# Kernel tuning notes

Measured on AMD Instinct MI355X. Metric: run time of the kernel, lower is better.

Reference implementation:

```python
import jax, jax.numpy as jnp
import numpy as np

B, N, C, K = 8, 4096, 128, 20  # batch, points-per-cloud, channels (n_cout), knn neighbors
NEG_SLOPE = 0.01  # torch F.leaky_relu default


def setup_inputs() -> dict:
    key = jax.random.key(0)
    ks = jax.random.split(key, 6)
    s = 1.0 / np.sqrt(C).astype(np.float32)
    xyz = jax.random.normal(ks[0], (B, 3, N), jnp.float32)
    points = jax.random.normal(ks[1], (B, C, N), jnp.float32)
    Wc = jax.random.normal(ks[2], (C, C), jnp.float32) * s  # center 1x1 conv weight (out,in)
    bc = jax.random.normal(ks[3], (C,), jnp.float32) * s
    Wg = jax.random.normal(ks[4], (C, C), jnp.float32) * s  # grouped 1x1 conv weight
    bg = jax.random.normal(ks[5], (C,), jnp.float32) * s
    return {"xyz": xyz, "points": points, "Wc": Wc, "bc": bc, "Wg": Wg, "bg": bg}


def reference(xyz, points, Wc, bc, Wg, bg):
    # xyz: [B,3,N], points: [B,C,N]
    k = K
    shortcut = points
    p = jax.nn.leaky_relu(points, NEG_SLOPE)        # [B,C,N]
    pt = jnp.transpose(p, (0, 2, 1))                # [B,N,C]
    xt = jnp.transpose(xyz, (0, 2, 1))              # [B,N,3]

    # pairwise squared distances [B,N,N]
    sq_norm = jnp.sum(xt * xt, axis=-1)             # [B,N]
    sq = sq_norm[:, :, None] - 2.0 * jnp.einsum('bnd,bmd->bnm', xt, xt) + sq_norm[:, None, :]

    # knn: k+1 nearest (incl. self), drop self -> [B,N,k]
    _, idx = jax.lax.top_k(-sq, k + 1)
    idx = idx[:, :, 1:]

    # gather neighbor features: [B,N,k,C]
    grouped = jax.vmap(lambda a, i: a[i])(pt, idx)

    # center 1x1 conv on [B,C,1,N] == per-point linear
    center = jnp.einsum('oc,bcn->bon', Wc, p) + bc[None, :, None]      # [B,C,N]
    # grouped 1x1 conv on [B,C,k,N]
    gout = jnp.einsum('oc,bnkc->bokn', Wg, grouped) + bg[None, :, None, None]  # [B,C,k,N]

    # mean over concat([center(1), grouped(k)], axis=2) then residual
    pooled = (center + jnp.sum(gout, axis=2)) / (k + 1)
    return pooled + shortcut
```

## Files before the change

### kernel.cpp

```cpp
#include <hip/hip_runtime.h>

#define B 8
#define N 4096
#define C 128
#define C2 256
#define KNN 21
#define CAP 22

typedef unsigned long long u64;
typedef unsigned int u32;
typedef unsigned short u16;

typedef __attribute__((ext_vector_type(8))) short bf16x8;
typedef __attribute__((ext_vector_type(4))) float f32x4;

__device__ __forceinline__ float bf2f(u16 u) {
    return __uint_as_float(((u32)u) << 16);
}
__device__ __forceinline__ u16 f2bf(float f) {
    u32 x = __float_as_uint(f);
    return (u16)((x + 0x7FFFu + ((x >> 16) & 1u)) >> 16);
}

__global__ __launch_bounds__(256) void k_transpose_lrelu(
        const float* __restrict__ pts, u16* __restrict__ X) {
    __shared__ u16 tile[32][33];
    int b  = blockIdx.z;
    int c0 = blockIdx.y * 32;
    int n0 = blockIdx.x * 32;
    int tx = threadIdx.x, ty = threadIdx.y;
    const float* src = pts + (size_t)b * C * N;
    #pragma unroll
    for (int i = 0; i < 32; i += 8) {
        float v = src[(size_t)(c0 + ty + i) * N + n0 + tx];
        if (v < 0.f) v = __fmul_rn(v, 0.01f);
        tile[ty + i][tx] = f2bf(v);
    }
    __syncthreads();
    u16* dst = X + (size_t)b * N * C2;
    #pragma unroll
    for (int i = 0; i < 32; i += 8) {
        dst[(size_t)(n0 + ty + i) * C2 + (c0 + tx)] = tile[tx][ty + i];
    }
}

__global__ __launch_bounds__(256) void k_pack_w(
        const float* __restrict__ Wc, const float* __restrict__ Wg,
        u16* __restrict__ Wt) {
    int e = blockIdx.x * 256 + threadIdx.x;
    int o = e >> 8, c = e & 255;
    float v = (c < 128) ? Wc[o * 128 + c] : Wg[o * 128 + (c - 128)];
    Wt[e] = f2bf(v);
}

__global__ __launch_bounds__(256) void k_knn_gather(
        const float* __restrict__ xyz, u16* __restrict__ X) {
    __shared__ __align__(16) char lds[61440];
    float4* stg = (float4*)lds;
    u64*    buf = (u64*)(lds + 16384);
    u64*    mg  = (u64*)lds;
    __shared__ u16 win[64 * KNN];

    int tid = threadIdx.x;
    int w = tid >> 6, l = tid & 63;
    int b = blockIdx.y;
    int n0 = blockIdx.x * 64;
    int nq = n0 + l;

    const float* xz = xyz + (size_t)b * 3 * N;
    float qx = xz[nq], qy = xz[N + nq], qz = xz[2 * N + nq];
    float snq = __fadd_rn(__fadd_rn(__fmul_rn(qx, qx), __fmul_rn(qy, qy)),
                          __fmul_rn(qz, qz));

    u64 slot[KNN];
    #pragma unroll
    for (int i = 0; i < KNN; ++i) slot[i] = ~0ull;
    int cnt = 0;
    u32 thr_kb = 0xFFFFFFFFu;
    float4* mystg = stg + w * 256;

    auto compact = [&]() {
        #pragma unroll 1
        for (int i = 0; i < CAP; ++i) {
            if (__ballot(i < cnt) == 0ull) break;
            u64 item = buf[i * 256 + tid];
            bool ins = (i < cnt) && (item < slot[20]);
            if (__ballot(ins) != 0ull) {
                u64 cnd = ins ? item : ~0ull;
                slot[20] = cnd < slot[20] ? cnd : slot[20];
                #pragma unroll
                for (int t = 19; t >= 0; --t) {
                    u64 a = slot[t], bb = slot[t + 1];
                    u64 lo = a < bb ? a : bb;
                    u64 hi = a < bb ? bb : a;
                    slot[t] = lo; slot[t + 1] = hi;
                }
            }
        }
        cnt = 0;
        thr_kb = (u32)(slot[20] >> 32);
    };

    for (int sc = 0; sc < 4; ++sc) {
        int m0 = w * 1024 + sc * 256;
        #pragma unroll
        for (int r = 0; r < 4; ++r) {
            int j = l + 64 * r, m = m0 + j;
            float x = xz[m], y = xz[N + m], z = xz[2 * N + m];
            float sn = __fadd_rn(__fadd_rn(__fmul_rn(x, x), __fmul_rn(y, y)),
                                 __fmul_rn(z, z));
            mystg[j] = make_float4(x, y, z, sn);
        }
        asm volatile("s_waitcnt lgkmcnt(0)" ::: "memory");
        for (int cc = 0; cc < 256; cc += 8) {
            #pragma unroll
            for (int j = 0; j < 8; ++j) {
                float4 cp = mystg[cc + j];
                int m = m0 + cc + j;
                float dot = __fadd_rn(__fadd_rn(__fmul_rn(qx, cp.x),
                                                __fmul_rn(qy, cp.y)),
                                      __fmul_rn(qz, cp.z));
                float sq = __fadd_rn(__fsub_rn(snq, __fadd_rn(dot, dot)), cp.w);
                u32 bits = __float_as_uint(sq);
                u32 kb = bits ^ (0x80000000u | (u32)(((int)bits) >> 31));
                buf[cnt * 256 + tid] = ((u64)kb << 32) | (u32)m;
                cnt += (kb <= thr_kb);
            }
            if (__ballot(cnt >= 15) != 0ull) compact();
        }
    }
    compact();

    __syncthreads();
    #pragma unroll
    for (int j = 0; j < KNN; ++j) mg[(w * 64 + l) * KNN + j] = slot[j];
    __syncthreads();

    if (w == 0) {
        int p0 = 0, p1 = 0, p2 = 0, p3 = 0;
        for (int j = 0; j < KNN; ++j) {
            u64 c0 = mg[(0 * 64 + l) * KNN + p0];
            u64 c1 = mg[(1 * 64 + l) * KNN + p1];
            u64 c2 = mg[(2 * 64 + l) * KNN + p2];
            u64 c3 = mg[(3 * 64 + l) * KNN + p3];
            u64 m01 = c0 < c1 ? c0 : c1; int s01 = c0 < c1 ? 0 : 1;
            u64 m23 = c2 < c3 ? c2 : c3; int s23 = c2 < c3 ? 2 : 3;
            u64 mm = m01 < m23 ? m01 : m23;
            int sel = m01 < m23 ? s01 : s23;
            win[l * KNN + j] = (u16)(mm & 0xFFFFu);
            p0 += (sel == 0); p1 += (sel == 1); p2 += (sel == 2); p3 += (sel == 3);
        }
    }
    __syncthreads();

    const u16* Xb = X + (size_t)b * N * C2;
    for (int qq = 0; qq < 16; ++qq) {
        int q = w * 16 + qq;
        float f0 = 0.f, f1 = 0.f;
        for (int j = 1; j < KNN; ++j) {
            int m = win[q * KNN + j];
            u32 u2 = *(const u32*)(Xb + (size_t)m * C2 + 2 * l);
            f0 += bf2f((u16)(u2 & 0xFFFFu));
            f1 += bf2f((u16)(u2 >> 16));
        }
        u16* dst = X + ((size_t)b * N + n0 + q) * C2 + 128 + 2 * l;
        *(u32*)dst = ((u32)f2bf(f1) << 16) | (u32)f2bf(f0);
    }
}

__global__ __launch_bounds__(256) void k_gemm_mfma(
        const u16* __restrict__ X, const u16* __restrict__ Wt,
        const float* __restrict__ pts, const float* __restrict__ bc,
        const float* __restrict__ bg, float* __restrict__ out) {
    int wid = blockIdx.x * 4 + (threadIdx.x >> 6);
    int lane = threadIdx.x & 63;
    int ot = wid & 7;
    int nt = wid >> 3;
    int b  = nt >> 6;
    int n0 = (nt & 63) * 64;

    int l16 = lane & 15, lq = lane >> 4;
    const u16* Xb = X + (size_t)b * N * C2;
    const u16* aptr = Wt + (size_t)(ot * 16 + l16) * C2 + lq * 8;
    const u16* bptr0 = Xb + (size_t)(n0 + 0 * 16 + l16) * C2 + lq * 8;
    const u16* bptr1 = Xb + (size_t)(n0 + 1 * 16 + l16) * C2 + lq * 8;
    const u16* bptr2 = Xb + (size_t)(n0 + 2 * 16 + l16) * C2 + lq * 8;
    const u16* bptr3 = Xb + (size_t)(n0 + 3 * 16 + l16) * C2 + lq * 8;

    f32x4 acc0 = {0.f, 0.f, 0.f, 0.f};
    f32x4 acc1 = {0.f, 0.f, 0.f, 0.f};
    f32x4 acc2 = {0.f, 0.f, 0.f, 0.f};
    f32x4 acc3 = {0.f, 0.f, 0.f, 0.f};
    #pragma unroll
    for (int kk = 0; kk < 8; ++kk) {
        bf16x8 a  = *(const bf16x8*)(aptr  + kk * 32);
        bf16x8 b0 = *(const bf16x8*)(bptr0 + kk * 32);
        bf16x8 b1 = *(const bf16x8*)(bptr1 + kk * 32);
        bf16x8 b2 = *(const bf16x8*)(bptr2 + kk * 32);
        bf16x8 b3 = *(const bf16x8*)(bptr3 + kk * 32);
        acc0 = __builtin_amdgcn_mfma_f32_16x16x32_bf16(a, b0, acc0, 0, 0, 0);
        acc1 = __builtin_amdgcn_mfma_f32_16x16x32_bf16(a, b1, acc1, 0, 0, 0);
        acc2 = __builtin_amdgcn_mfma_f32_16x16x32_bf16(a, b2, acc2, 0, 0, 0);
        acc3 = __builtin_amdgcn_mfma_f32_16x16x32_bf16(a, b3, acc3, 0, 0, 0);
    }

    const float inv21 = 1.0f / 21.0f;
    float bias[4];
    #pragma unroll
    for (int r = 0; r < 4; ++r) {
        int o = ot * 16 + lq * 4 + r;
        bias[r] = bc[o] + 20.f * bg[o];
    }
    const float* pb = pts + (size_t)b * C * N;
    float* ob = out + (size_t)b * C * N;
    f32x4 accs[4] = {acc0, acc1, acc2, acc3};
    #pragma unroll
    for (int t = 0; t < 4; ++t) {
        int n = n0 + t * 16 + l16;
        #pragma unroll
        for (int r = 0; r < 4; ++r) {
            int o = ot * 16 + lq * 4 + r;
            ob[(size_t)o * N + n] =
                (accs[t][r] + bias[r]) * inv21 + pb[(size_t)o * N + n];
        }
    }
}

extern "C" void kernel_launch(void* const* d_in, const int* in_sizes, int n_in,
                              void* d_out, int out_size, void* d_ws, size_t ws_size,
                              hipStream_t stream) {
    const float* xyz = (const float*)d_in[0];
    const float* pts = (const float*)d_in[1];
    const float* Wc  = (const float*)d_in[2];
    const float* bc  = (const float*)d_in[3];
    const float* Wg  = (const float*)d_in[4];
    const float* bg  = (const float*)d_in[5];
    float* out = (float*)d_out;

    char* ws = (char*)d_ws;
    u16* X  = (u16*)ws;
    u16* Wt = (u16*)(ws + (size_t)B * N * C2 * 2);

    k_transpose_lrelu<<<dim3(N / 32, C / 32, B), dim3(32, 8), 0, stream>>>(pts, X);
    k_pack_w<<<dim3(128), dim3(256), 0, stream>>>(Wc, Wg, Wt);
    k_knn_gather<<<dim3(N / 64, B), dim3(256), 0, stream>>>(xyz, X);
    k_gemm_mfma<<<dim3(1024), dim3(256), 0, stream>>>(X, Wt, pts, bc, bg, out);
}
```

Measured before the change: 306.0 us.

## Split kNN candidate buffer into key/index arrays and fold weight packing into GEMM

Candidate buffers in the kNN kernel now store 32-bit keys and 16-bit indices separately, and the top-k sorting network tracks keys and indices as parallel u32 arrays. This shrinks shared memory per block, potentially allowing more resident blocks, and reduces staging store width. The separate weight-packing kernel is removed; the GEMM converts fp32 weights to bf16 on the fly, saving a launch. The candidate filter becomes strict, which changes tie handling, and the gather loop is unrolled.

```diff
diff --git a/kernel.cpp b/kernel.cpp
--- a/kernel.cpp
+++ b/kernel.cpp
@@ -44,21 +44,13 @@
     }
 }
 
-__global__ __launch_bounds__(256) void k_pack_w(
-        const float* __restrict__ Wc, const float* __restrict__ Wg,
-        u16* __restrict__ Wt) {
-    int e = blockIdx.x * 256 + threadIdx.x;
-    int o = e >> 8, c = e & 255;
-    float v = (c < 128) ? Wc[o * 128 + c] : Wg[o * 128 + (c - 128)];
-    Wt[e] = f2bf(v);
-}
-
 __global__ __launch_bounds__(256) void k_knn_gather(
         const float* __restrict__ xyz, u16* __restrict__ X) {
-    __shared__ __align__(16) char lds[61440];
-    float4* stg = (float4*)lds;
-    u64*    buf = (u64*)(lds + 16384);
-    u64*    mg  = (u64*)lds;
+    __shared__ __align__(16) char lds[50176];
+    float4* stg  = (float4*)lds;
+    u32*    kbuf = (u32*)(lds + 16384);
+    u16*    ibuf = (u16*)(lds + 16384 + 22528);
+    u64*    mg   = (u64*)lds;
     __shared__ u16 win[64 * KNN];
 
     int tid = threadIdx.x;
@@ -72,33 +64,37 @@
     float snq = __fadd_rn(__fadd_rn(__fmul_rn(qx, qx), __fmul_rn(qy, qy)),
                           __fmul_rn(qz, qz));
 
-    u64 slot[KNN];
-    #pragma unroll
-    for (int i = 0; i < KNN; ++i) slot[i] = ~0ull;
+    u32 key[KNN], idx[KNN];
+    #pragma unroll
+    for (int i = 0; i < KNN; ++i) { key[i] = 0xFFFFFFFFu; idx[i] = 0u; }
     int cnt = 0;
-    u32 thr_kb = 0xFFFFFFFFu;
+    u32 thr = 0xFFFFFFFFu;
     float4* mystg = stg + w * 256;
 
     auto compact = [&]() {
         #pragma unroll 1
         for (int i = 0; i < CAP; ++i) {
             if (__ballot(i < cnt) == 0ull) break;
-            u64 item = buf[i * 256 + tid];
-            bool ins = (i < cnt) && (item < slot[20]);
+            u32 kv = kbuf[i * 256 + tid];
+            u32 iv = ibuf[i * 256 + tid];
+            bool ins = (i < cnt) && (kv < key[20]);
             if (__ballot(ins) != 0ull) {
-                u64 cnd = ins ? item : ~0ull;
-                slot[20] = cnd < slot[20] ? cnd : slot[20];
+                key[20] = ins ? kv : key[20];
+                idx[20] = ins ? iv : idx[20];
                 #pragma unroll
                 for (int t = 19; t >= 0; --t) {
-                    u64 a = slot[t], bb = slot[t + 1];
-                    u64 lo = a < bb ? a : bb;
-                    u64 hi = a < bb ? bb : a;
-                    slot[t] = lo; slot[t + 1] = hi;
+                    bool sw = key[t] > key[t + 1];
+                    u32 ka = sw ? key[t + 1] : key[t];
+                    u32 kz = sw ? key[t] : key[t + 1];
+                    u32 ia = sw ? idx[t + 1] : idx[t];
+                    u32 iz = sw ? idx[t] : idx[t + 1];
+                    key[t] = ka; key[t + 1] = kz;
+                    idx[t] = ia; idx[t + 1] = iz;
                 }
             }
         }
         cnt = 0;
-        thr_kb = (u32)(slot[20] >> 32);
+        thr = key[20];
     };
 
     for (int sc = 0; sc < 4; ++sc) {
@@ -123,8 +119,9 @@
                 float sq = __fadd_rn(__fsub_rn(snq, __fadd_rn(dot, dot)), cp.w);
                 u32 bits = __float_as_uint(sq);
                 u32 kb = bits ^ (0x80000000u | (u32)(((int)bits) >> 31));
-                buf[cnt * 256 + tid] = ((u64)kb << 32) | (u32)m;
-                cnt += (kb <= thr_kb);
+                kbuf[cnt * 256 + tid] = kb;
+                ibuf[cnt * 256 + tid] = (u16)m;
+                cnt += (kb < thr);
             }
             if (__ballot(cnt >= 15) != 0ull) compact();
         }
@@ -133,7 +130,8 @@
 
     __syncthreads();
     #pragma unroll
-    for (int j = 0; j < KNN; ++j) mg[(w * 64 + l) * KNN + j] = slot[j];
+    for (int j = 0; j < KNN; ++j)
+        mg[(w * 64 + l) * KNN + j] = ((u64)key[j] << 32) | (u64)idx[j];
     __syncthreads();
 
     if (w == 0) {
@@ -157,6 +155,7 @@
     for (int qq = 0; qq < 16; ++qq) {
         int q = w * 16 + qq;
         float f0 = 0.f, f1 = 0.f;
+        #pragma unroll
         for (int j = 1; j < KNN; ++j) {
             int m = win[q * KNN + j];
             u32 u2 = *(const u32*)(Xb + (size_t)m * C2 + 2 * l);
@@ -169,9 +168,10 @@
 }
 
 __global__ __launch_bounds__(256) void k_gemm_mfma(
-        const u16* __restrict__ X, const u16* __restrict__ Wt,
-        const float* __restrict__ pts, const float* __restrict__ bc,
-        const float* __restrict__ bg, float* __restrict__ out) {
+        const u16* __restrict__ X, const float* __restrict__ Wc,
+        const float* __restrict__ Wg, const float* __restrict__ pts,
+        const float* __restrict__ bc, const float* __restrict__ bg,
+        float* __restrict__ out) {
     int wid = blockIdx.x * 4 + (threadIdx.x >> 6);
     int lane = threadIdx.x & 63;
     int ot = wid & 7;
@@ -181,11 +181,12 @@
 
     int l16 = lane & 15, lq = lane >> 4;
     const u16* Xb = X + (size_t)b * N * C2;
-    const u16* aptr = Wt + (size_t)(ot * 16 + l16) * C2 + lq * 8;
     const u16* bptr0 = Xb + (size_t)(n0 + 0 * 16 + l16) * C2 + lq * 8;
     const u16* bptr1 = Xb + (size_t)(n0 + 1 * 16 + l16) * C2 + lq * 8;
     const u16* bptr2 = Xb + (size_t)(n0 + 2 * 16 + l16) * C2 + lq * 8;
     const u16* bptr3 = Xb + (size_t)(n0 + 3 * 16 + l16) * C2 + lq * 8;
+    const float* wrowc = Wc + (size_t)(ot * 16 + l16) * 128 + lq * 8;
+    const float* wrowg = Wg + (size_t)(ot * 16 + l16) * 128 + lq * 8;
 
     f32x4 acc0 = {0.f, 0.f, 0.f, 0.f};
     f32x4 acc1 = {0.f, 0.f, 0.f, 0.f};
@@ -193,7 +194,14 @@
     f32x4 acc3 = {0.f, 0.f, 0.f, 0.f};
     #pragma unroll
     for (int kk = 0; kk < 8; ++kk) {
-        bf16x8 a  = *(const bf16x8*)(aptr  + kk * 32);
+        const float* ws = (kk < 4) ? (wrowc + kk * 32) : (wrowg + (kk - 4) * 32);
+        float4 wa = *(const float4*)ws;
+        float4 wb = *(const float4*)(ws + 4);
+        bf16x8 a;
+        a[0] = (short)f2bf(wa.x); a[1] = (short)f2bf(wa.y);
+        a[2] = (short)f2bf(wa.z); a[3] = (short)f2bf(wa.w);
+        a[4] = (short)f2bf(wb.x); a[5] = (short)f2bf(wb.y);
+        a[6] = (short)f2bf(wb.z); a[7] = (short)f2bf(wb.w);
         bf16x8 b0 = *(const bf16x8*)(bptr0 + kk * 32);
         bf16x8 b1 = *(const bf16x8*)(bptr1 + kk * 32);
         bf16x8 b2 = *(const bf16x8*)(bptr2 + kk * 32);
@@ -237,12 +245,9 @@
     const float* bg  = (const float*)d_in[5];
     float* out = (float*)d_out;
 
-    char* ws = (char*)d_ws;
-    u16* X  = (u16*)ws;
-    u16* Wt = (u16*)(ws + (size_t)B * N * C2 * 2);
+    u16* X = (u16*)d_ws;
 
     k_transpose_lrelu<<<dim3(N / 32, C / 32, B), dim3(32, 8), 0, stream>>>(pts, X);
-    k_pack_w<<<dim3(128), dim3(256), 0, stream>>>(Wc, Wg, Wt);
     k_knn_gather<<<dim3(N / 64, B), dim3(256), 0, stream>>>(xyz, X);
-    k_gemm_mfma<<<dim3(1024), dim3(256), 0, stream>>>(X, Wt, pts, bc, bg, out);
-}
+    k_gemm_mfma<<<dim3(1024), dim3(256), 0, stream>>>(X, Wc, Wg, pts, bc, bg, out);
+}
```

Measured after the change: 285.7 us. -6.6%, faster.
